# Performance work log

Measured on AMD Instinct MI355X. Metric: run time of the kernel, lower is better.

The kernel has to match this reference:

```python
import jax, jax.numpy as jnp
import numpy as np

IN_FEATURES = 4096
OUT_FEATURES = 16384

def setup_inputs() -> dict:
    key = jax.random.key(0)
    k_x, k_w = jax.random.split(key, 2)
    x = jax.random.normal(k_x, (2, 2048, IN_FEATURES), dtype=jnp.float32)
    # quantized uint8 weight stored as int32 (values in [0, 255])
    weight_idx = jax.random.randint(k_w, (OUT_FEATURES, IN_FEATURES), 0, 256, dtype=jnp.int32)
    # per-tensor quantization params (buffers in the original module)
    scale = jnp.float32(0.0123)
    zp = jnp.float32(128.0)
    bias = jnp.zeros((OUT_FEATURES,), dtype=jnp.float32)
    return {"x": x, "weight_idx": weight_idx, "scale": scale, "zp": zp, "bias": bias}

def reference(x, weight_idx, scale, zp, bias):
    # dequantize: w = (q - zp) * scale, shape [out, in]
    w = (weight_idx.astype(jnp.float32) - zp) * scale
    # F.linear: x @ w.T + bias
    return jnp.einsum('bsi,oi->bso', x, w) + bias
```

## Files before the change

kernel.cpp:

```cpp
#include <hip/hip_runtime.h>
#include <stdint.h>
#include <stddef.h>

#define MDIM 4096
#define NDIM 16384
#define KDIM 4096

typedef __bf16 bf16;
typedef __bf16 bf16x8 __attribute__((ext_vector_type(8)));
typedef float  fx4    __attribute__((ext_vector_type(4)));
typedef int    ix4    __attribute__((ext_vector_type(4)));

#define AS1(p) ((const __attribute__((address_space(1))) void*)(p))
#define AS3(p) ((__attribute__((address_space(3))) void*)(p))

__global__ __launch_bounds__(256) void cvt_x_kernel(const fx4* __restrict__ x,
                                                    bf16x8* __restrict__ xb, int n8) {
    int i = blockIdx.x * 256 + threadIdx.x;
    if (i < n8) {
        fx4 v0 = x[2 * i];
        fx4 v1 = x[2 * i + 1];
        bf16x8 o;
        o[0] = (bf16)v0[0]; o[1] = (bf16)v0[1]; o[2] = (bf16)v0[2]; o[3] = (bf16)v0[3];
        o[4] = (bf16)v1[0]; o[5] = (bf16)v1[1]; o[6] = (bf16)v1[2]; o[7] = (bf16)v1[3];
        xb[i] = o;
    }
}

__global__ __launch_bounds__(256) void cvt_w_kernel(const ix4* __restrict__ q,
                                                    bf16x8* __restrict__ wb,
                                                    const float* __restrict__ zp_ptr, int n8) {
    float zp = *zp_ptr;
    int i = blockIdx.x * 256 + threadIdx.x;
    if (i < n8) {
        ix4 v0 = q[2 * i];
        ix4 v1 = q[2 * i + 1];
        bf16x8 o;
        o[0] = (bf16)((float)v0[0] - zp); o[1] = (bf16)((float)v0[1] - zp);
        o[2] = (bf16)((float)v0[2] - zp); o[3] = (bf16)((float)v0[3] - zp);
        o[4] = (bf16)((float)v1[0] - zp); o[5] = (bf16)((float)v1[1] - zp);
        o[6] = (bf16)((float)v1[2] - zp); o[7] = (bf16)((float)v1[3] - zp);
        wb[i] = o;
    }
}

__global__ __launch_bounds__(256) void gemm_kernel(const bf16* __restrict__ A,
                                                   const bf16* __restrict__ B,
                                                   const float* __restrict__ scale_ptr,
                                                   const float* __restrict__ bias,
                                                   float* __restrict__ C) {
    constexpr int BK = 32;
    __shared__ bf16 As[128 * BK];
    __shared__ bf16 Bs[128 * BK];

    const int tid  = threadIdx.x;
    const int wave = tid >> 6;
    const int lane = tid & 63;

    const int bn = blockIdx.x;
    const int bm = blockIdx.y;

    const int rowStage  = wave * 32 + (lane >> 2);
    const int srcChunk  = (lane & 3) ^ ((lane >> 3) & 3);
    const int kStage    = srcChunk * 8;
    const bf16* aptr0 = A + (size_t)(bm * 128 + rowStage) * KDIM + kStage;
    const bf16* aptr1 = aptr0 + 16 * KDIM;
    const bf16* bptr0 = B + (size_t)(bn * 128 + rowStage) * KDIM + kStage;
    const bf16* bptr1 = bptr0 + 16 * KDIM;
    bf16* AsW = As + wave * 1024;
    bf16* BsW = Bs + wave * 1024;

    const int wm = (wave >> 1) * 64;
    const int wn = (wave & 1) * 64;
    const int fr = lane & 15;
    const int fq = lane >> 4;
    const int sw = (fr >> 1) & 3;
    const bf16* aRead = As + (wm + fr) * BK + (fq ^ sw) * 8;
    const bf16* bRead = Bs + (wn + fr) * BK + (fq ^ sw) * 8;

    fx4 acc[4][4];
#pragma unroll
    for (int mi = 0; mi < 4; ++mi)
#pragma unroll
        for (int ni = 0; ni < 4; ++ni)
            acc[mi][ni] = fx4{0.f, 0.f, 0.f, 0.f};

    const int KT = KDIM / BK;
    for (int kt = 0; kt < KT; ++kt) {
        __syncthreads();
        __builtin_amdgcn_global_load_lds(AS1(aptr0), AS3(AsW),       16, 0, 0);
        __builtin_amdgcn_global_load_lds(AS1(aptr1), AS3(AsW + 512), 16, 0, 0);
        __builtin_amdgcn_global_load_lds(AS1(bptr0), AS3(BsW),       16, 0, 0);
        __builtin_amdgcn_global_load_lds(AS1(bptr1), AS3(BsW + 512), 16, 0, 0);
        aptr0 += BK; aptr1 += BK; bptr0 += BK; bptr1 += BK;
        __syncthreads();

        bf16x8 af[4], bfr[4];
#pragma unroll
        for (int i = 0; i < 4; ++i) {
            af[i]  = *(const bf16x8*)(aRead + i * 16 * BK);
            bfr[i] = *(const bf16x8*)(bRead + i * 16 * BK);
        }
#pragma unroll
        for (int mi = 0; mi < 4; ++mi)
#pragma unroll
            for (int ni = 0; ni < 4; ++ni)
                acc[mi][ni] = __builtin_amdgcn_mfma_f32_16x16x32_bf16(af[mi], bfr[ni], acc[mi][ni], 0, 0, 0);
    }

    const float s = *scale_ptr;
    float bv[4];
#pragma unroll
    for (int ni = 0; ni < 4; ++ni)
        bv[ni] = bias[bn * 128 + wn + ni * 16 + fr];

    const int c0 = bn * 128 + wn + fr;
    const int r0 = bm * 128 + wm + fq * 4;
#pragma unroll
    for (int mi = 0; mi < 4; ++mi) {
#pragma unroll
        for (int i = 0; i < 4; ++i) {
            float* crow = C + (size_t)(r0 + mi * 16 + i) * NDIM + c0;
#pragma unroll
            for (int ni = 0; ni < 4; ++ni)
                crow[ni * 16] = s * acc[mi][ni][i] + bv[ni];
        }
    }
}

__global__ __launch_bounds__(256) void naive_kernel(const float* __restrict__ x,
                                                    const int* __restrict__ q,
                                                    const float* __restrict__ sp,
                                                    const float* __restrict__ zpp,
                                                    const float* __restrict__ bias,
                                                    float* __restrict__ out) {
    float s = *sp, zp = *zpp;
    size_t idx = (size_t)blockIdx.x * 256 + threadIdx.x;
    int m = (int)(idx / NDIM);
    int n = (int)(idx % NDIM);
    const fx4* xr = (const fx4*)(x + (size_t)m * KDIM);
    const ix4* qr = (const ix4*)(q + (size_t)n * KDIM);
    float acc = 0.f;
    for (int k = 0; k < KDIM / 4; ++k) {
        fx4 xv = xr[k];
        ix4 qv = qr[k];
        acc += xv[0] * ((float)qv[0] - zp) + xv[1] * ((float)qv[1] - zp)
             + xv[2] * ((float)qv[2] - zp) + xv[3] * ((float)qv[3] - zp);
    }
    out[idx] = s * acc + bias[n];
}

extern "C" void kernel_launch(void* const* d_in, const int* in_sizes, int n_in,
                              void* d_out, int out_size, void* d_ws, size_t ws_size,
                              hipStream_t stream) {
    const float* x     = (const float*)d_in[0];
    const int*   q     = (const int*)d_in[1];
    const float* scale = (const float*)d_in[2];
    const float* zp    = (const float*)d_in[3];
    const float* bias  = (const float*)d_in[4];
    float* out = (float*)d_out;

    const size_t need = ((size_t)MDIM * KDIM + (size_t)NDIM * KDIM) * sizeof(bf16);
    if (ws_size >= need) {
        bf16* xb = (bf16*)d_ws;
        bf16* wb = xb + (size_t)MDIM * KDIM;

        const int nx8 = MDIM * KDIM / 8;
        const int nw8 = NDIM * KDIM / 8;
        cvt_x_kernel<<<nx8 / 256, 256, 0, stream>>>((const fx4*)x, (bf16x8*)xb, nx8);
        cvt_w_kernel<<<nw8 / 256, 256, 0, stream>>>((const ix4*)q, (bf16x8*)wb, zp, nw8);

        dim3 grid(NDIM / 128, MDIM / 128);
        gemm_kernel<<<grid, 256, 0, stream>>>(xb, wb, scale, bias, out);
    } else {
        naive_kernel<<<((size_t)MDIM * NDIM) / 256, 256, 0, stream>>>(x, q, scale, zp, bias, out);
    }
}
```

Before: 1.092 ms.

## Use 256x256 tiles with double-buffered async LDS pipeline and block swizzle

Rewrites the GEMM kernel to use 256x256 output tiles with 512 threads (8 waves, each computing 128x64). It double-buffers LDS with two K-halves per buffer and issues the next global-to-LDS loads before computing on the current buffer, using vmcnt waits and barriers. It also remaps block IDs for L2 locality and raises MFMA priority around the compute. The aim is to hide global load latency and raise arithmetic intensity, at the cost of 128KB of LDS and higher register pressure.

```diff
diff --git a/kernel.cpp b/kernel.cpp
--- a/kernel.cpp
+++ b/kernel.cpp
@@ -44,80 +44,124 @@
     }
 }
 
-__global__ __launch_bounds__(256) void gemm_kernel(const bf16* __restrict__ A,
-                                                   const bf16* __restrict__ B,
-                                                   const float* __restrict__ scale_ptr,
-                                                   const float* __restrict__ bias,
-                                                   float* __restrict__ C) {
-    constexpr int BK = 32;
-    __shared__ bf16 As[128 * BK];
-    __shared__ bf16 Bs[128 * BK];
+__global__ __launch_bounds__(512, 2) void gemm_kernel(const bf16* __restrict__ A,
+                                                      const bf16* __restrict__ B,
+                                                      const float* __restrict__ scale_ptr,
+                                                      const float* __restrict__ bias,
+                                                      float* __restrict__ C) {
+    __shared__ bf16 As[2 * 2 * 8192];
+    __shared__ bf16 Bs[2 * 2 * 8192];
 
     const int tid  = threadIdx.x;
     const int wave = tid >> 6;
     const int lane = tid & 63;
 
-    const int bn = blockIdx.x;
-    const int bm = blockIdx.y;
-
-    const int rowStage  = wave * 32 + (lane >> 2);
-    const int srcChunk  = (lane & 3) ^ ((lane >> 3) & 3);
-    const int kStage    = srcChunk * 8;
-    const bf16* aptr0 = A + (size_t)(bm * 128 + rowStage) * KDIM + kStage;
-    const bf16* aptr1 = aptr0 + 16 * KDIM;
-    const bf16* bptr0 = B + (size_t)(bn * 128 + rowStage) * KDIM + kStage;
-    const bf16* bptr1 = bptr0 + 16 * KDIM;
-    bf16* AsW = As + wave * 1024;
-    bf16* BsW = Bs + wave * 1024;
-
-    const int wm = (wave >> 1) * 64;
-    const int wn = (wave & 1) * 64;
+    const int bid = blockIdx.x;
+    const int swz = (bid & 7) * 128 + (bid >> 3);
+    const int bm = swz >> 6;
+    const int bn = swz & 63;
+
+    const int rowS   = wave * 32 + (lane >> 2);
+    const int gChunk = (lane & 3) ^ ((lane >> 3) & 3);
+    const bf16* aS0 = A + (size_t)(bm * 256 + rowS) * KDIM + gChunk * 8;
+    const bf16* aS1 = aS0 + (size_t)16 * KDIM;
+    const bf16* bS0 = B + (size_t)(bn * 256 + rowS) * KDIM + gChunk * 8;
+    const bf16* bS1 = bS0 + (size_t)16 * KDIM;
+    const int ldsW0 = wave * 1024;
+    const int ldsW1 = wave * 1024 + 512;
+
+    const int wm = wave >> 2;
+    const int wn = wave & 3;
     const int fr = lane & 15;
     const int fq = lane >> 4;
     const int sw = (fr >> 1) & 3;
-    const bf16* aRead = As + (wm + fr) * BK + (fq ^ sw) * 8;
-    const bf16* bRead = Bs + (wn + fr) * BK + (fq ^ sw) * 8;
-
-    fx4 acc[4][4];
-#pragma unroll
-    for (int mi = 0; mi < 4; ++mi)
+    const int aOff = (wm * 128 + fr) * 32 + ((fq ^ sw) * 8);
+    const int bOff = (wn * 64  + fr) * 32 + ((fq ^ sw) * 8);
+
+    fx4 acc[8][4];
+#pragma unroll
+    for (int mi = 0; mi < 8; ++mi)
 #pragma unroll
         for (int ni = 0; ni < 4; ++ni)
             acc[mi][ni] = fx4{0.f, 0.f, 0.f, 0.f};
 
-    const int KT = KDIM / BK;
-    for (int kt = 0; kt < KT; ++kt) {
-        __syncthreads();
-        __builtin_amdgcn_global_load_lds(AS1(aptr0), AS3(AsW),       16, 0, 0);
-        __builtin_amdgcn_global_load_lds(AS1(aptr1), AS3(AsW + 512), 16, 0, 0);
-        __builtin_amdgcn_global_load_lds(AS1(bptr0), AS3(BsW),       16, 0, 0);
-        __builtin_amdgcn_global_load_lds(AS1(bptr1), AS3(BsW + 512), 16, 0, 0);
-        aptr0 += BK; aptr1 += BK; bptr0 += BK; bptr1 += BK;
-        __syncthreads();
-
-        bf16x8 af[4], bfr[4];
-#pragma unroll
-        for (int i = 0; i < 4; ++i) {
-            af[i]  = *(const bf16x8*)(aRead + i * 16 * BK);
-            bfr[i] = *(const bf16x8*)(bRead + i * 16 * BK);
-        }
-#pragma unroll
-        for (int mi = 0; mi < 4; ++mi)
-#pragma unroll
-            for (int ni = 0; ni < 4; ++ni)
-                acc[mi][ni] = __builtin_amdgcn_mfma_f32_16x16x32_bf16(af[mi], bfr[ni], acc[mi][ni], 0, 0, 0);
-    }
+#define STAGE(bufSel, kh, kg) do {                                                        \
+    const int _o = (bufSel) * 16384 + (kh) * 8192;                                        \
+    __builtin_amdgcn_global_load_lds(AS1(aS0 + (kg)), AS3(As + _o + ldsW0), 16, 0, 0);    \
+    __builtin_amdgcn_global_load_lds(AS1(aS1 + (kg)), AS3(As + _o + ldsW1), 16, 0, 0);    \
+    __builtin_amdgcn_global_load_lds(AS1(bS0 + (kg)), AS3(Bs + _o + ldsW0), 16, 0, 0);    \
+    __builtin_amdgcn_global_load_lds(AS1(bS1 + (kg)), AS3(Bs + _o + ldsW1), 16, 0, 0);    \
+} while (0)
+
+#define COMPUTE(bufSel, kh) do {                                                          \
+    const bf16* _aB = As + (bufSel) * 16384 + (kh) * 8192 + aOff;                         \
+    const bf16* _bB = Bs + (bufSel) * 16384 + (kh) * 8192 + bOff;                         \
+    bf16x8 af[8], bfr[4];                                                                 \
+    _Pragma("unroll")                                                                     \
+    for (int mi = 0; mi < 8; ++mi) af[mi] = *(const bf16x8*)(_aB + mi * 512);             \
+    _Pragma("unroll")                                                                     \
+    for (int ni = 0; ni < 4; ++ni) bfr[ni] = *(const bf16x8*)(_bB + ni * 512);            \
+    __builtin_amdgcn_s_setprio(1);                                                        \
+    _Pragma("unroll")                                                                     \
+    for (int mi = 0; mi < 8; ++mi)                                                        \
+        _Pragma("unroll")                                                                 \
+        for (int ni = 0; ni < 4; ++ni)                                                    \
+            acc[mi][ni] = __builtin_amdgcn_mfma_f32_16x16x32_bf16(af[mi], bfr[ni],        \
+                                                                  acc[mi][ni], 0, 0, 0); \
+    __builtin_amdgcn_s_setprio(0);                                                        \
+} while (0)
+
+#define PHASE_S(bufR, kh, kgNext) do {                                                    \
+    STAGE((bufR) ^ 1, kh, kgNext);                                                        \
+    asm volatile("s_waitcnt vmcnt(8)" ::: "memory");                                      \
+    __builtin_amdgcn_s_barrier();                                                         \
+    __builtin_amdgcn_sched_barrier(0);                                                    \
+    COMPUTE(bufR, kh);                                                                    \
+    __builtin_amdgcn_sched_barrier(0);                                                    \
+    __builtin_amdgcn_s_barrier();                                                         \
+} while (0)
+
+    STAGE(0, 0, 0);
+    STAGE(0, 1, 32);
+
+    for (int t = 0; t < 62; t += 2) {
+        const int kg = t * 64;
+        PHASE_S(0, 0, kg + 64);
+        PHASE_S(0, 1, kg + 96);
+        PHASE_S(1, 0, kg + 128);
+        PHASE_S(1, 1, kg + 160);
+    }
+    {
+        PHASE_S(0, 0, 4032);
+        PHASE_S(0, 1, 4064);
+    }
+    asm volatile("s_waitcnt vmcnt(4)" ::: "memory");
+    __builtin_amdgcn_s_barrier();
+    __builtin_amdgcn_sched_barrier(0);
+    COMPUTE(1, 0);
+    __builtin_amdgcn_sched_barrier(0);
+    __builtin_amdgcn_s_barrier();
+    asm volatile("s_waitcnt vmcnt(0)" ::: "memory");
+    __builtin_amdgcn_s_barrier();
+    __builtin_amdgcn_sched_barrier(0);
+    COMPUTE(1, 1);
+
+#undef PHASE_S
+#undef COMPUTE
+#undef STAGE
+
+    asm volatile("" ::: "memory");
 
     const float s = *scale_ptr;
     float bv[4];
 #pragma unroll
     for (int ni = 0; ni < 4; ++ni)
-        bv[ni] = bias[bn * 128 + wn + ni * 16 + fr];
-
-    const int c0 = bn * 128 + wn + fr;
-    const int r0 = bm * 128 + wm + fq * 4;
-#pragma unroll
-    for (int mi = 0; mi < 4; ++mi) {
+        bv[ni] = bias[bn * 256 + wn * 64 + ni * 16 + fr];
+
+    const int c0 = bn * 256 + wn * 64 + fr;
+    const int r0 = bm * 256 + wm * 128 + fq * 4;
+#pragma unroll
+    for (int mi = 0; mi < 8; ++mi) {
 #pragma unroll
         for (int i = 0; i < 4; ++i) {
             float* crow = C + (size_t)(r0 + mi * 16 + i) * NDIM + c0;
@@ -170,8 +214,8 @@
         cvt_x_kernel<<<nx8 / 256, 256, 0, stream>>>((const fx4*)x, (bf16x8*)xb, nx8);
         cvt_w_kernel<<<nw8 / 256, 256, 0, stream>>>((const ix4*)q, (bf16x8*)wb, zp, nw8);
 
-        dim3 grid(NDIM / 128, MDIM / 128);
-        gemm_kernel<<<grid, 256, 0, stream>>>(xb, wb, scale, bias, out);
+        dim3 grid((NDIM / 256) * (MDIM / 256));
+        gemm_kernel<<<grid, 512, 0, stream>>>(xb, wb, scale, bias, out);
     } else {
         naive_kernel<<<((size_t)MDIM * NDIM) / 256, 256, 0, stream>>>(x, q, scale, zp, bias, out);
     }
```

Result: faster. 1.043 ms (-4.5%).
